# Performance work log

Measured on AMD Instinct MI355X. Metric: run time of the kernel, lower is better.

The kernel has to match this reference:

```python
import jax, jax.numpy as jnp
import numpy as np

# 'tetra_chiral' permutation table from the original module
_TETRA_CHIRAL = np.array([
    [0, 1, 2, 3], [0, 2, 3, 1], [0, 3, 1, 2], [1, 0, 3, 2],
    [1, 2, 0, 3], [1, 3, 2, 0], [2, 0, 1, 3], [2, 1, 3, 0],
    [2, 3, 0, 1], [3, 0, 2, 1], [3, 1, 0, 2], [3, 2, 1, 0]], dtype=np.int32)

N, H = 65536, 256
BN_EPS = 1e-5


def setup_inputs() -> dict:
    key = jax.random.key(0)
    ks = jax.random.split(key, 6)
    x = jax.random.normal(ks[0], (N, 4, H), dtype=jnp.float32)
    # 4 hidden x hidden linears (xavier-ish scale), stacked [4, H, H] (torch weight layout: [out, in])
    Wb = jax.random.normal(ks[1], (4, H, H), dtype=jnp.float32) * (1.0 / np.sqrt(H))
    bb = jnp.zeros((4, H), dtype=jnp.float32)
    W1 = jax.random.normal(ks[2], (H, H), dtype=jnp.float32) * (1.0 / np.sqrt(H))
    b1 = jnp.zeros((H,), dtype=jnp.float32)
    gamma = jnp.ones((H,), dtype=jnp.float32)
    beta = jnp.zeros((H,), dtype=jnp.float32)
    W2 = jax.random.normal(ks[3], (H, H), dtype=jnp.float32) * (1.0 / np.sqrt(H))
    b2 = jnp.zeros((H,), dtype=jnp.float32)
    perms = jnp.asarray(_TETRA_CHIRAL)
    return {"x": x, "Wb": Wb, "bb": bb, "W1": W1, "b1": b1,
            "gamma": gamma, "beta": beta, "W2": W2, "b2": b2, "perms": perms}


def reference(x, Wb, bb, W1, b1, gamma, beta, W2, b2, perms):
    # x: [N, 4, H]; perms: [P, 4] with P=12 (tetra_chiral)
    # For each permutation p: relu(sum_k tanh(Linear_k(x[:, p[k], :]))), accumulated over p.
    acc = jnp.zeros((x.shape[0], perms.shape[0], x.shape[2]), dtype=x.dtype)  # [N, P, H]
    for k in range(4):  # fixed tiny loop over the 4 slot-linears
        xs = x[:, perms[:, k], :]  # gather: [N, P, H]
        acc = acc + jnp.tanh(jnp.einsum('nph,gh->npg', xs, Wb[k]) + bb[k])
    nei = jnp.maximum(acc, 0.0).sum(axis=1)  # relu per perm, sum over perms -> [N, H]
    # mlp_out: Linear -> BatchNorm1d(eval: mean=0, var=1) -> ReLU -> Linear
    z = (nei / 3.0) @ W1.T + b1
    inv = jnp.float32(1.0 / np.sqrt(1.0 + BN_EPS))
    h = jnp.maximum(z * inv * gamma + beta, 0.0)
    return h @ W2.T + b2
```

## Files before the change

kernel.cpp:

```cpp
#include <hip/hip_runtime.h>
#include <cstdint>
#include <cstddef>

typedef __bf16 bf16x8 __attribute__((ext_vector_type(8)));
typedef float  f32x16 __attribute__((ext_vector_type(16)));

__device__ __forceinline__ unsigned f2bf_u(float f){
  unsigned u = __float_as_uint(f);
  return (u + 0x7FFFu + ((u >> 16) & 1u)) >> 16;
}
__device__ __forceinline__ unsigned short f2bf(float f){ return (unsigned short)f2bf_u(f); }
__device__ __forceinline__ unsigned pk2(float a, float b){ return f2bf_u(a) | (f2bf_u(b) << 16); }

__device__ __forceinline__ float fast_tanh(float x){
  float xx = fminf(fmaxf(x, -8.0f), 8.0f);
  float e  = __builtin_amdgcn_exp2f(xx * 2.8853900817779268f);
  return 1.0f - 2.0f * __builtin_amdgcn_rcpf(e + 1.0f);
}

#define MFMA(a,b,c) __builtin_amdgcn_mfma_f32_32x32x16_bf16((a),(b),(c),0,0,0)

__device__ __forceinline__ void ld_lds16(const void* g, void* l){
  __builtin_amdgcn_global_load_lds(
      (const __attribute__((address_space(1))) unsigned int*)g,
      (__attribute__((address_space(3))) unsigned int*)l, 16, 0, 0);
}
__device__ __forceinline__ bf16x8 mk_frag(uint2 lo, uint2 hi){
  return __builtin_bit_cast(bf16x8, make_uint4(lo.x, lo.y, hi.x, hi.y));
}

__global__ void prep_wb(const float* __restrict__ Wb, unsigned short* __restrict__ dst){
  int s  = blockIdx.x*256 + threadIdx.x;
  int r  = s & 31;
  int c  = (s>>5) & 3;
  int tj = (s>>7) & 3;
  int ks = (s>>9) & 3;
  int kq = (s>>11) & 3;
  int gc = (s>>13) & 7;
  const float* src = Wb + ((size_t)tj*256 + gc*32 + r)*256 + kq*64 + ks*16 + c*4;
  float4 f = *reinterpret_cast<const float4*>(src);
  ushort4 o; o.x=f2bf(f.x); o.y=f2bf(f.y); o.z=f2bf(f.z); o.w=f2bf(f.w);
  *reinterpret_cast<ushort4*>(dst + (size_t)s*4) = o;
}

__global__ void prep_w(const float* __restrict__ W1, const float* __restrict__ W2,
                       unsigned short* __restrict__ dst){
  int id = blockIdx.x*256 + threadIdx.x;
  const float* W = (id < 8192) ? W1 : W2;
  int s  = id & 8191;
  int l  = s & 63;
  int ks = (s>>6) & 15;
  int ct = (s>>10) & 7;
  const float* src = W + ((size_t)ct*32 + (l&31))*256 + ks*16 + (l>>5)*8;
  float4 f0 = *reinterpret_cast<const float4*>(src);
  float4 f1 = *reinterpret_cast<const float4*>(src + 4);
  ushort4 a, b;
  a.x=f2bf(f0.x); a.y=f2bf(f0.y); a.z=f2bf(f0.z); a.w=f2bf(f0.w);
  b.x=f2bf(f1.x); b.y=f2bf(f1.y); b.z=f2bf(f1.z); b.w=f2bf(f1.w);
  ushort4* d = reinterpret_cast<ushort4*>(dst + (size_t)id*8);
  d[0] = a; d[1] = b;
}

__launch_bounds__(256, 3)
__global__ void tetra_main(const float* __restrict__ x,
                           const float* __restrict__ bb,
                           const float* __restrict__ b1,
                           const float* __restrict__ gam,
                           const float* __restrict__ bet,
                           const float* __restrict__ b2,
                           const unsigned short* __restrict__ wsWb,
                           const unsigned short* __restrict__ wsW1,
                           const unsigned short* __restrict__ wsW2,
                           float* __restrict__ out)
{
  __shared__ __align__(16) uint2 sbuf[2][2048];
  __shared__ __align__(16) uint2 snei[2048];

  constexpr int PT[12][4] = {{0,1,2,3},{0,2,3,1},{0,3,1,2},{1,0,3,2},{1,2,0,3},{1,3,2,0},
                             {2,0,1,3},{2,1,3,0},{2,3,0,1},{3,0,2,1},{3,1,0,2},{3,2,1,0}};

  const int tid  = threadIdx.x;
  const int w    = tid >> 6;
  const int lane = tid & 63;
  const int l31  = lane & 31;
  const int q    = lane >> 5;

  uint4 fragA[16];
  {
    const float* arow = x + ((size_t)blockIdx.x*128 + (size_t)(w*32 + l31))*256 + q*8;
#pragma unroll
    for (int s = 0; s < 16; ++s){
      float4 f0 = *reinterpret_cast<const float4*>(arow + s*16);
      float4 f1 = *reinterpret_cast<const float4*>(arow + s*16 + 4);
      fragA[s] = make_uint4(pk2(f0.x,f0.y), pk2(f0.z,f0.w), pk2(f1.x,f1.y), pk2(f1.z,f1.w));
    }
  }

  auto stage = [&](int t){
    const char* g = (const char*)wsWb + (size_t)t*16384 + w*4096 + lane*16;
    char* lb = (char*)(&sbuf[t&1][0]) + w*4096;
#pragma unroll
    for (int i = 0; i < 4; ++i)
      ld_lds16(g + i*1024, lb + i*1024);
  };

  stage(0);

  unsigned short* sn = (unsigned short*)snei;
  int t = 0;
  for (int gc = 0; gc < 8; ++gc){
    f32x16 acc[4];
#pragma unroll
    for (int k = 0; k < 4; ++k)
#pragma unroll
      for (int r = 0; r < 16; ++r) acc[k][r] = 0.0f;

#pragma unroll
    for (int kq = 0; kq < 4; ++kq, ++t){
      __syncthreads();
      if (t < 31) stage(t+1);
      const uint2* B = sbuf[t&1];
      const int boff = q*64 + l31;
#pragma unroll
      for (int ks = 0; ks < 4; ++ks){
        bf16x8 av = __builtin_bit_cast(bf16x8, fragA[kq*4 + ks]);
#pragma unroll
        for (int tj = 0; tj < 4; ++tj){
          int idx = (ks*16 + tj*4)*32 + boff;
          uint2 lo = B[idx], hi = B[idx + 32];
          acc[tj] = MFMA(av, mk_frag(lo, hi), acc[tj]);
        }
      }
    }

    const int g0 = gc*32;
#pragma unroll
    for (int k = 0; k < 4; ++k){
      float bbv = bb[k*256 + g0 + l31];
#pragma unroll
      for (int r = 0; r < 16; ++r)
        acc[k][r] = fast_tanh(acc[k][r] + bbv);
    }
    const int col   = g0 + l31;
    const int sbase = (col>>2)*128 + (col&3);
#pragma unroll
    for (int nb = 0; nb < 4; ++nb){
      float s = 0.0f;
#pragma unroll
      for (int p = 0; p < 12; ++p){
        float v = acc[0][nb*4 + PT[p][0]] + acc[1][nb*4 + PT[p][1]]
                + acc[2][nb*4 + PT[p][2]] + acc[3][nb*4 + PT[p][3]];
        s += fmaxf(v, 0.0f);
      }
      sn[sbase + (w*8 + 2*nb + q)*4] = f2bf(s * (1.0f/3.0f));
    }
  }

  __syncthreads();

  const int ct0 = w*2, ct1 = w*2 + 1;
  f32x16 a2[2];
#pragma unroll
  for (int j = 0; j < 2; ++j)
#pragma unroll
    for (int r = 0; r < 16; ++r) a2[j][r] = 0.0f;
  {
    const uint4* W1f = (const uint4*)wsW1;
    uint4 bp[8][2];
#pragma unroll
    for (int i = 0; i < 8; ++i){
      bp[i][0] = W1f[(ct0*16 + i)*64 + lane];
      bp[i][1] = W1f[(ct1*16 + i)*64 + lane];
    }
#pragma unroll
    for (int ks = 0; ks < 16; ++ks){
      int ai = (ks*4 + q*2)*32 + l31;
      uint2 lo = snei[ai], hi = snei[ai + 32];
      bf16x8 av = mk_frag(lo, hi);
      uint4 c0 = bp[ks&7][0], c1 = bp[ks&7][1];
      if (ks < 8){
        bp[ks][0] = W1f[(ct0*16 + ks + 8)*64 + lane];
        bp[ks][1] = W1f[(ct1*16 + ks + 8)*64 + lane];
      }
      a2[0] = MFMA(av, __builtin_bit_cast(bf16x8, c0), a2[0]);
      a2[1] = MFMA(av, __builtin_bit_cast(bf16x8, c1), a2[1]);
    }
  }
  __syncthreads();
  {
    const float inv = 0.9999950000374998f;
#pragma unroll
    for (int tj = 0; tj < 2; ++tj){
      int col = (w*2 + tj)*32 + l31;
      float b1v = b1[col], gv = gam[col], btv = bet[col];
#pragma unroll
      for (int r = 0; r < 16; ++r){
        int row = (r&3) + 8*(r>>2) + 4*q;
        float z  = a2[tj][r] + b1v;
        sn[(col>>2)*128 + row*4 + (col&3)] = f2bf(fmaxf(z*inv*gv + btv, 0.0f));
      }
    }
  }
  __syncthreads();

  f32x16 a3[2];
#pragma unroll
  for (int j = 0; j < 2; ++j)
#pragma unroll
    for (int r = 0; r < 16; ++r) a3[j][r] = 0.0f;
  {
    const uint4* W2f = (const uint4*)wsW2;
    uint4 bp[8][2];
#pragma unroll
    for (int i = 0; i < 8; ++i){
      bp[i][0] = W2f[(ct0*16 + i)*64 + lane];
      bp[i][1] = W2f[(ct1*16 + i)*64 + lane];
    }
#pragma unroll
    for (int ks = 0; ks < 16; ++ks){
      int ai = (ks*4 + q*2)*32 + l31;
      uint2 lo = snei[ai], hi = snei[ai + 32];
      bf16x8 av = mk_frag(lo, hi);
      uint4 c0 = bp[ks&7][0], c1 = bp[ks&7][1];
      if (ks < 8){
        bp[ks][0] = W2f[(ct0*16 + ks + 8)*64 + lane];
        bp[ks][1] = W2f[(ct1*16 + ks + 8)*64 + lane];
      }
      a3[0] = MFMA(av, __builtin_bit_cast(bf16x8, c0), a3[0]);
      a3[1] = MFMA(av, __builtin_bit_cast(bf16x8, c1), a3[1]);
    }
  }
#pragma unroll
  for (int tj = 0; tj < 2; ++tj){
    int col = (w*2 + tj)*32 + l31;
    float b2v = b2[col];
#pragma unroll
    for (int r = 0; r < 16; ++r){
      int row = (r&3) + 8*(r>>2) + 4*q;
      out[((size_t)blockIdx.x*32 + row)*256 + col] = a3[tj][r] + b2v;
    }
  }
}

extern "C" void kernel_launch(void* const* d_in, const int* in_sizes, int n_in,
                              void* d_out, int out_size, void* d_ws, size_t ws_size,
                              hipStream_t stream)
{
  (void)n_in; (void)out_size; (void)ws_size;
  const float* x   = (const float*)d_in[0];
  const float* Wb  = (const float*)d_in[1];
  const float* bb  = (const float*)d_in[2];
  const float* W1  = (const float*)d_in[3];
  const float* b1  = (const float*)d_in[4];
  const float* gam = (const float*)d_in[5];
  const float* bet = (const float*)d_in[6];
  const float* W2  = (const float*)d_in[7];
  const float* b2  = (const float*)d_in[8];
  float* out = (float*)d_out;

  unsigned short* wsWb = (unsigned short*)d_ws;
  unsigned short* wsW1 = wsWb + 262144;
  unsigned short* wsW2 = wsW1 + 65536;

  prep_wb<<<dim3(256), dim3(256), 0, stream>>>(Wb, wsWb);
  prep_w <<<dim3(64),  dim3(256), 0, stream>>>(W1, W2, wsW1);

  const int N = in_sizes[0] / (4*256);
  tetra_main<<<dim3(N/32), dim3(256), 0, stream>>>(x, bb, b1, gam, bet, b2,
                                                   wsWb, wsW1, wsW2, out);
}
```

Baseline: 547.5 us.

## Repack weight and activation LDS layouts for 128-bit fragment loads, fold bias into accumulator

Reorders the bf16 Wb staging layout so each MFMA B fragment is a single 16-byte LDS read rather than two 8-byte reads. The hidden-activation LDS buffer becomes a padded row-major array so A fragments also load as one 128-bit read. The bias is prefetched one group ahead and used to initialise the accumulators, and the tanh clamp is dropped. The main cost targeted is LDS instruction count and bank conflicts in the inner MFMA loops. Removing the clamp relies on exp2/rcp saturating cleanly for large inputs.

```diff
diff --git a/kernel.cpp b/kernel.cpp
--- a/kernel.cpp
+++ b/kernel.cpp
@@ -13,9 +13,8 @@
 __device__ __forceinline__ unsigned pk2(float a, float b){ return f2bf_u(a) | (f2bf_u(b) << 16); }
 
 __device__ __forceinline__ float fast_tanh(float x){
-  float xx = fminf(fmaxf(x, -8.0f), 8.0f);
-  float e  = __builtin_amdgcn_exp2f(xx * 2.8853900817779268f);
-  return 1.0f - 2.0f * __builtin_amdgcn_rcpf(e + 1.0f);
+  float e = __builtin_amdgcn_exp2f(x * 2.8853900817779268f);
+  return __builtin_fmaf(-2.0f, __builtin_amdgcn_rcpf(e + 1.0f), 1.0f);
 }
 
 #define MFMA(a,b,c) __builtin_amdgcn_mfma_f32_32x32x16_bf16((a),(b),(c),0,0,0)
@@ -25,22 +24,22 @@
       (const __attribute__((address_space(1))) unsigned int*)g,
       (__attribute__((address_space(3))) unsigned int*)l, 16, 0, 0);
 }
-__device__ __forceinline__ bf16x8 mk_frag(uint2 lo, uint2 hi){
-  return __builtin_bit_cast(bf16x8, make_uint4(lo.x, lo.y, hi.x, hi.y));
-}
 
 __global__ void prep_wb(const float* __restrict__ Wb, unsigned short* __restrict__ dst){
-  int s  = blockIdx.x*256 + threadIdx.x;
-  int r  = s & 31;
-  int c  = (s>>5) & 3;
-  int tj = (s>>7) & 3;
-  int ks = (s>>9) & 3;
-  int kq = (s>>11) & 3;
-  int gc = (s>>13) & 7;
-  const float* src = Wb + ((size_t)tj*256 + gc*32 + r)*256 + kq*64 + ks*16 + c*4;
-  float4 f = *reinterpret_cast<const float4*>(src);
-  ushort4 o; o.x=f2bf(f.x); o.y=f2bf(f.y); o.z=f2bf(f.z); o.w=f2bf(f.w);
-  *reinterpret_cast<ushort4*>(dst + (size_t)s*4) = o;
+  int s   = blockIdx.x*256 + threadIdx.x;
+  int u   = s & 1023;
+  int t   = s >> 10;
+  int col = u & 31;
+  int q   = (u>>5) & 1;
+  int tj  = (u>>6) & 3;
+  int ks  = (u>>8) & 3;
+  int kq  = t & 3;
+  int gc  = t >> 2;
+  const float* src = Wb + ((size_t)(tj*256 + gc*32 + col))*256 + kq*64 + ks*16 + q*8;
+  float4 f0 = *reinterpret_cast<const float4*>(src);
+  float4 f1 = *reinterpret_cast<const float4*>(src + 4);
+  uint4 o = make_uint4(pk2(f0.x,f0.y), pk2(f0.z,f0.w), pk2(f1.x,f1.y), pk2(f1.z,f1.w));
+  *reinterpret_cast<uint4*>(dst + (size_t)s*8) = o;
 }
 
 __global__ void prep_w(const float* __restrict__ W1, const float* __restrict__ W2,
@@ -54,11 +53,8 @@
   const float* src = W + ((size_t)ct*32 + (l&31))*256 + ks*16 + (l>>5)*8;
   float4 f0 = *reinterpret_cast<const float4*>(src);
   float4 f1 = *reinterpret_cast<const float4*>(src + 4);
-  ushort4 a, b;
-  a.x=f2bf(f0.x); a.y=f2bf(f0.y); a.z=f2bf(f0.z); a.w=f2bf(f0.w);
-  b.x=f2bf(f1.x); b.y=f2bf(f1.y); b.z=f2bf(f1.z); b.w=f2bf(f1.w);
-  ushort4* d = reinterpret_cast<ushort4*>(dst + (size_t)id*8);
-  d[0] = a; d[1] = b;
+  uint4 o = make_uint4(pk2(f0.x,f0.y), pk2(f0.z,f0.w), pk2(f1.x,f1.y), pk2(f1.z,f1.w));
+  *reinterpret_cast<uint4*>(dst + (size_t)id*8) = o;
 }
 
 __launch_bounds__(256, 3)
@@ -73,8 +69,9 @@
                            const unsigned short* __restrict__ wsW2,
                            float* __restrict__ out)
 {
-  __shared__ __align__(16) uint2 sbuf[2][2048];
-  __shared__ __align__(16) uint2 snei[2048];
+  constexpr int NSTR = 264;
+  __shared__ __align__(16) unsigned char smem[32768];
+  __shared__ __align__(16) unsigned short snei[32*NSTR + 8];
 
   constexpr int PT[12][4] = {{0,1,2,3},{0,2,3,1},{0,3,1,2},{1,0,3,2},{1,2,0,3},{1,3,2,0},
                              {2,0,1,3},{2,1,3,0},{2,3,0,1},{3,0,2,1},{3,1,0,2},{3,2,1,0}};
@@ -97,8 +94,8 @@
   }
 
   auto stage = [&](int t){
-    const char* g = (const char*)wsWb + (size_t)t*16384 + w*4096 + lane*16;
-    char* lb = (char*)(&sbuf[t&1][0]) + w*4096;
+    const char* g = (const char*)wsWb + ((size_t)t<<14) + (w<<12) + lane*16;
+    char* lb = (char*)smem + ((t&1)<<14) + (w<<12);
 #pragma unroll
     for (int i = 0; i < 4; ++i)
       ld_lds16(g + i*1024, lb + i*1024);
@@ -106,43 +103,49 @@
 
   stage(0);
 
-  unsigned short* sn = (unsigned short*)snei;
+  float bbn[4];
+#pragma unroll
+  for (int k = 0; k < 4; ++k) bbn[k] = bb[k*256 + l31];
+
   int t = 0;
   for (int gc = 0; gc < 8; ++gc){
+    float bbv[4];
+#pragma unroll
+    for (int k = 0; k < 4; ++k) bbv[k] = bbn[k];
+    if (gc < 7){
+#pragma unroll
+      for (int k = 0; k < 4; ++k) bbn[k] = bb[k*256 + (gc+1)*32 + l31];
+    }
+
     f32x16 acc[4];
 #pragma unroll
     for (int k = 0; k < 4; ++k)
 #pragma unroll
-      for (int r = 0; r < 16; ++r) acc[k][r] = 0.0f;
+      for (int r = 0; r < 16; ++r) acc[k][r] = bbv[k];
 
 #pragma unroll
     for (int kq = 0; kq < 4; ++kq, ++t){
       __syncthreads();
       if (t < 31) stage(t+1);
-      const uint2* B = sbuf[t&1];
-      const int boff = q*64 + l31;
+      const uint4* Bq = (const uint4*)(smem + ((t&1)<<14)) + q*32 + l31;
 #pragma unroll
       for (int ks = 0; ks < 4; ++ks){
         bf16x8 av = __builtin_bit_cast(bf16x8, fragA[kq*4 + ks]);
 #pragma unroll
         for (int tj = 0; tj < 4; ++tj){
-          int idx = (ks*16 + tj*4)*32 + boff;
-          uint2 lo = B[idx], hi = B[idx + 32];
-          acc[tj] = MFMA(av, mk_frag(lo, hi), acc[tj]);
+          bf16x8 bv = __builtin_bit_cast(bf16x8, Bq[(ks*4 + tj)*64]);
+          acc[tj] = MFMA(av, bv, acc[tj]);
         }
       }
     }
 
-    const int g0 = gc*32;
-#pragma unroll
-    for (int k = 0; k < 4; ++k){
-      float bbv = bb[k*256 + g0 + l31];
+#pragma unroll
+    for (int k = 0; k < 4; ++k)
 #pragma unroll
       for (int r = 0; r < 16; ++r)
-        acc[k][r] = fast_tanh(acc[k][r] + bbv);
-    }
-    const int col   = g0 + l31;
-    const int sbase = (col>>2)*128 + (col&3);
+        acc[k][r] = fast_tanh(acc[k][r]);
+
+    const int cb = gc*32 + l31;
 #pragma unroll
     for (int nb = 0; nb < 4; ++nb){
       float s = 0.0f;
@@ -152,7 +155,7 @@
                 + acc[2][nb*4 + PT[p][2]] + acc[3][nb*4 + PT[p][3]];
         s += fmaxf(v, 0.0f);
       }
-      sn[sbase + (w*8 + 2*nb + q)*4] = f2bf(s * (1.0f/3.0f));
+      snei[(w*8 + 2*nb + q)*NSTR + cb] = f2bf(s * (1.0f/3.0f));
     }
   }
 
@@ -174,9 +177,7 @@
     }
 #pragma unroll
     for (int ks = 0; ks < 16; ++ks){
-      int ai = (ks*4 + q*2)*32 + l31;
-      uint2 lo = snei[ai], hi = snei[ai + 32];
-      bf16x8 av = mk_frag(lo, hi);
+      bf16x8 av = *reinterpret_cast<const bf16x8*>(&snei[l31*NSTR + ks*16 + q*8]);
       uint4 c0 = bp[ks&7][0], c1 = bp[ks&7][1];
       if (ks < 8){
         bp[ks][0] = W1f[(ct0*16 + ks + 8)*64 + lane];
@@ -197,7 +198,7 @@
       for (int r = 0; r < 16; ++r){
         int row = (r&3) + 8*(r>>2) + 4*q;
         float z  = a2[tj][r] + b1v;
-        sn[(col>>2)*128 + row*4 + (col&3)] = f2bf(fmaxf(z*inv*gv + btv, 0.0f));
+        snei[row*NSTR + col] = f2bf(fmaxf(z*inv*gv + btv, 0.0f));
       }
     }
   }
@@ -218,9 +219,7 @@
     }
 #pragma unroll
     for (int ks = 0; ks < 16; ++ks){
-      int ai = (ks*4 + q*2)*32 + l31;
-      uint2 lo = snei[ai], hi = snei[ai + 32];
-      bf16x8 av = mk_frag(lo, hi);
+      bf16x8 av = *reinterpret_cast<const bf16x8*>(&snei[l31*NSTR + ks*16 + q*8]);
       uint4 c0 = bp[ks&7][0], c1 = bp[ks&7][1];
       if (ks < 8){
         bp[ks][0] = W2f[(ct0*16 + ks + 8)*64 + lane];
@@ -262,7 +261,7 @@
   unsigned short* wsW1 = wsWb + 262144;
   unsigned short* wsW2 = wsW1 + 65536;
 
-  prep_wb<<<dim3(256), dim3(256), 0, stream>>>(Wb, wsWb);
+  prep_wb<<<dim3(128), dim3(256), 0, stream>>>(Wb, wsWb);
   prep_w <<<dim3(64),  dim3(256), 0, stream>>>(W1, W2, wsW1);
 
   const int N = in_sizes[0] / (4*256);
```

After: 553.4 us. Within noise of the previous version (+1.1%).
